# Kernel tuning notes

Measured on AMD Instinct MI355X. Metric: run time of the kernel, lower is better.

The kernel has to match this reference:

```python
import jax, jax.numpy as jnp
import numpy as np
from jax import lax

B, CIN, COUT, K = 256, 3, 16, 3
D, H, W_ = 16, 32, 32
POOL = 4


def setup_inputs() -> dict:
    key = jax.random.key(0)
    kx, kw, kb = jax.random.split(key, 3)
    x = jax.random.normal(kx, (B, CIN, D, H, W_), dtype=jnp.float32)
    # Conv3d default init scale ~ 1/sqrt(fan_in)
    fan_in = CIN * K * K * K
    bound = 1.0 / np.sqrt(fan_in)
    W = jax.random.uniform(kw, (COUT, CIN, K, K, K), dtype=jnp.float32, minval=-bound, maxval=bound)
    b = jax.random.uniform(kb, (COUT,), dtype=jnp.float32, minval=-bound, maxval=bound)
    return {"x": x, "W": W, "b": b}


def reference(x, W, b):
    # Conv3d, valid padding, stride 1: [B,16,14,30,30]
    y = lax.conv_general_dilated(
        x, W, window_strides=(1, 1, 1), padding="VALID",
        dimension_numbers=("NCDHW", "OIDHW", "NCDHW"))
    y = y + b[None, :, None, None, None]
    # channel softmax (dim=1)
    s = jax.nn.softmax(y, axis=1)
    # 4x4x4 max-pool, stride 4, no padding: [B,16,3,7,7]
    out = lax.reduce_window(
        s, -jnp.inf, lax.max,
        window_dimensions=(1, 1, POOL, POOL, POOL),
        window_strides=(1, 1, POOL, POOL, POOL),
        padding="VALID")
    return out
```

## Files before the change

### kernel.cpp

```cpp
#include <hip/hip_runtime.h>
#include <math.h>

#define BATCH 256
#define CIN   3
#define COUT  16
#define DI    16
#define HI    32
#define WI    32

typedef _Float16 f16;
typedef f16   f16x4 __attribute__((ext_vector_type(4)));
typedef f16   f16x8 __attribute__((ext_vector_type(8)));
typedef float f32x4 __attribute__((ext_vector_type(4)));

#define LOG2E 1.44269504088896340736f

#define ROWU   144
#define PLANEU 4320
#define XS_N   (6 * PLANEU)
#define G8OFF  (2 * PLANEU + 2 * ROWU)

#define SV8(a, b) __builtin_shufflevector(a, b, 0, 1, 2, 3, 4, 5, 6, 7)
#define MFMA16(A, B, C) __builtin_amdgcn_mfma_f32_16x16x32_f16(A, B, C, 0, 0, 0)

#define DPPMAX(v, ctrl) do {                                                  \
    int t_ = __builtin_amdgcn_update_dpp(                                     \
        0, __builtin_bit_cast(int, v), (ctrl), 0xF, 0xF, false);              \
    v = fmaxf(v, __builtin_bit_cast(float, t_));                              \
} while (0)

__global__ __launch_bounds__(640, 8) void conv_sm_pool_mfma(
    const float* __restrict__ x, const float* __restrict__ W,
    const float* __restrict__ bias, float* __restrict__ out)
{
    __shared__ __align__(16) f16 xs[XS_N];

    const int tid  = threadIdx.x;
    const int lane = tid & 63;
    const int wave = tid >> 6;
    const int b    = blockIdx.x / 3;
    const int pd   = blockIdx.x % 3;
    const int d0   = pd * 4;

    const int col = lane & 15;
    const int kq  = lane >> 4;

    const float* wc  = W + col * 81;
    const float* wqp = wc + kq * 6;
    f16x8 wm[3];
    #pragma unroll
    for (int kw = 0; kw < 3; ++kw) {
        #pragma unroll
        for (int j = 0; j < 8; ++j) {
            const int ci = j & 3, jj = j >> 2;
            float v = (ci < 3) ? wqp[ci * 27 + 3 * jj + kw] * LOG2E : 0.f;
            wm[kw][j] = (f16)v;
        }
    }
    f16x8 wg = {};
    if (kq == 0) {
        #pragma unroll
        for (int j = 0; j < 8; ++j) {
            const int ci = j & 3, kw = j >> 2;
            if (ci < 3) wg[j] = (f16)(wc[ci * 27 + 24 + kw] * LOG2E);
        }
    } else if (kq == 1) {
        #pragma unroll
        for (int j = 0; j < 3; ++j) wg[j] = (f16)(wc[j * 27 + 26] * LOG2E);
    }
    const float4 braw = *(const float4*)(bias + kq * 4);
    float4 bv;
    bv.x = braw.x * LOG2E; bv.y = braw.y * LOG2E;
    bv.z = braw.z * LOG2E; bv.w = braw.w * LOG2E;

    for (int i = tid; i < 1440; i += 640) {
        int wqd = i & 7;
        int r   = i >> 3;
        int hh  = r % 30;
        int dd  = r / 30;
        const float* px = x + ((size_t)b * 48 + (d0 + dd)) * 1024 + hh * 32 + wqd * 4;
        float4 a0 = *(const float4*)(px);
        float4 a1 = *(const float4*)(px + 16384);
        float4 a2 = *(const float4*)(px + 32768);
        f16x8 p0, p1;
        p0[0] = (f16)a0.x; p0[1] = (f16)a1.x; p0[2] = (f16)a2.x; p0[3] = (f16)0.f;
        p0[4] = (f16)a0.y; p0[5] = (f16)a1.y; p0[6] = (f16)a2.y; p0[7] = (f16)0.f;
        p1[0] = (f16)a0.z; p1[1] = (f16)a1.z; p1[2] = (f16)a2.z; p1[3] = (f16)0.f;
        p1[4] = (f16)a0.w; p1[5] = (f16)a1.w; p1[6] = (f16)a2.w; p1[7] = (f16)0.f;
        f16* dst = xs + ((dd * 30 + hh) * 36 + wqd * 4) * 4;
        *(f16x8*)(dst)     = p0;
        *(f16x8*)(dst + 8) = p1;
    }

    const int g0   = kq * 2;
    const int off1 = (g0 / 3) * PLANEU + (g0 % 3) * ROWU;
    const int off2 = ((g0 + 1) / 3) * PLANEU + ((g0 + 1) % 3) * ROWU;
    const int hl = col >> 2, wl = col & 3;
    const int spat  = hl * ROWU + wl * 4;

    __syncthreads();

    for (int c = wave; c < 49; c += 10) {
        const int ch = c / 7;
        const int pw = c - ch * 7;
        const f16* base = xs + ch * 4 * ROWU + pw * 16 + spat;
        const f16* a1 = base + off1;
        const f16* a2 = base + off2;
        const f16* a3 = base + G8OFF;

        f32x4 acc[4];
        #pragma unroll
        for (int d = 0; d < 4; ++d) {
            const int dp = d * PLANEU;
            f16x4 b10 = *(const f16x4*)(a1 + dp);
            f16x4 b20 = *(const f16x4*)(a2 + dp);
            f16x4 b11 = *(const f16x4*)(a1 + dp + 4);
            f16x4 b21 = *(const f16x4*)(a2 + dp + 4);
            f16x4 b12 = *(const f16x4*)(a1 + dp + 8);
            f16x4 b22 = *(const f16x4*)(a2 + dp + 8);
            f16x4 ga = b10, gb = b11;
            if (kq == 0) {
                ga = *(const f16x4*)(a3 + dp);
                gb = *(const f16x4*)(a3 + dp + 4);
            } else if (kq == 1) {
                ga = *(const f16x4*)(a3 + dp + 8);
            }

            __builtin_amdgcn_s_setprio(1);
            f32x4 a_ = {0.f, 0.f, 0.f, 0.f};
            a_ = MFMA16(wm[0], SV8(b10, b20), a_);
            a_ = MFMA16(wm[1], SV8(b11, b21), a_);
            a_ = MFMA16(wm[2], SV8(b12, b22), a_);
            a_ = MFMA16(wg,    SV8(ga,  gb),  a_);
            __builtin_amdgcn_s_setprio(0);
            acc[d] = a_;
        }

        float ev[4][4], s[4];
        #pragma unroll
        for (int d = 0; d < 4; ++d) {
            float y0 = acc[d][0] + bv.x, y1 = acc[d][1] + bv.y;
            float y2 = acc[d][2] + bv.z, y3 = acc[d][3] + bv.w;
            ev[d][0] = __builtin_amdgcn_exp2f(y0);
            ev[d][1] = __builtin_amdgcn_exp2f(y1);
            ev[d][2] = __builtin_amdgcn_exp2f(y2);
            ev[d][3] = __builtin_amdgcn_exp2f(y3);
            s[d] = (ev[d][0] + ev[d][1]) + (ev[d][2] + ev[d][3]);
        }
        #pragma unroll
        for (int d = 0; d < 4; ++d) s[d] += __shfl_xor(s[d], 16);
        #pragma unroll
        for (int d = 0; d < 4; ++d) s[d] += __shfl_xor(s[d], 32);

        f32x4 pm = {0.f, 0.f, 0.f, 0.f};
        #pragma unroll
        for (int d = 0; d < 4; ++d) {
            float iv = __builtin_amdgcn_rcpf(s[d]);
            pm[0] = fmaxf(pm[0], ev[d][0] * iv);
            pm[1] = fmaxf(pm[1], ev[d][1] * iv);
            pm[2] = fmaxf(pm[2], ev[d][2] * iv);
            pm[3] = fmaxf(pm[3], ev[d][3] * iv);
        }

        #pragma unroll
        for (int r = 0; r < 4; ++r) {
            float v = pm[r];
            DPPMAX(v, 0x128);
            DPPMAX(v, 0x124);
            DPPMAX(v, 0x122);
            DPPMAX(v, 0x121);
            pm[r] = v;
        }

        if (col == 0) {
            float* po = out + ((size_t)b * COUT + kq * 4) * 147 + pd * 49 + c;
            po[0]   = pm[0];
            po[147] = pm[1];
            po[294] = pm[2];
            po[441] = pm[3];
        }
    }
}

extern "C" void kernel_launch(void* const* d_in, const int* in_sizes, int n_in,
                              void* d_out, int out_size, void* d_ws, size_t ws_size,
                              hipStream_t stream) {
    const float* x    = (const float*)d_in[0];
    const float* W    = (const float*)d_in[1];
    const float* bias = (const float*)d_in[2];
    float* out = (float*)d_out;

    conv_sm_pool_mfma<<<BATCH * 3, 640, 0, stream>>>(x, W, bias, out);
}
```

Before: 33.35 us.

## Split each block along H into two halves with 512 threads and smaller LDS

Each (batch, depth-slab) work item is now split into two workgroups covering output H rows 0-3 and 4-6, loading 18 or 14 input rows instead of 30. The LDS buffer shrinks, the block size drops to 512 threads, and the grid doubles. The intent is more resident blocks and better load balance across CUs, with a swizzled block index so paired halves land near each other. The change also drops the setprio hints and the kq-conditional loads for the extra MFMA operand, which now reads unconditionally. The cost is redundant halo loads (rows 16-17 are fetched by both halves) and more per-block setup.

```diff
diff --git a/kernel.cpp b/kernel.cpp
--- a/kernel.cpp
+++ b/kernel.cpp
@@ -16,7 +16,7 @@
 #define LOG2E 1.44269504088896340736f
 
 #define ROWU   144
-#define PLANEU 4320
+#define PLANEU (18 * ROWU)
 #define XS_N   (6 * PLANEU)
 #define G8OFF  (2 * PLANEU + 2 * ROWU)
 
@@ -29,7 +29,7 @@
     v = fmaxf(v, __builtin_bit_cast(float, t_));                              \
 } while (0)
 
-__global__ __launch_bounds__(640, 8) void conv_sm_pool_mfma(
+__global__ __launch_bounds__(512, 8) void conv_sm_pool_mfma(
     const float* __restrict__ x, const float* __restrict__ W,
     const float* __restrict__ bias, float* __restrict__ out)
 {
@@ -38,9 +38,15 @@
     const int tid  = threadIdx.x;
     const int lane = tid & 63;
     const int wave = tid >> 6;
-    const int b    = blockIdx.x / 3;
-    const int pd   = blockIdx.x % 3;
-    const int d0   = pd * 4;
+
+    const int wgid = blockIdx.x;
+    const int hc = (wgid >> 3) & 1;
+    const int p  = ((wgid >> 4) << 3) | (wgid & 7);
+    const int b  = p / 3;
+    const int pd = p % 3;
+    const int d0 = pd * 4;
+    const int row0  = hc ? 16 : 0;
+    const int nrows = hc ? 14 : 18;
 
     const int col = lane & 15;
     const int kq  = lane >> 4;
@@ -73,12 +79,14 @@
     bv.x = braw.x * LOG2E; bv.y = braw.y * LOG2E;
     bv.z = braw.z * LOG2E; bv.w = braw.w * LOG2E;
 
-    for (int i = tid; i < 1440; i += 640) {
+    const int nitems = 6 * nrows * 8;
+    for (int i = tid; i < nitems; i += 512) {
         int wqd = i & 7;
         int r   = i >> 3;
-        int hh  = r % 30;
-        int dd  = r / 30;
-        const float* px = x + ((size_t)b * 48 + (d0 + dd)) * 1024 + hh * 32 + wqd * 4;
+        int hh  = r % nrows;
+        int dd  = r / nrows;
+        const float* px = x + ((size_t)b * 48 + (d0 + dd)) * 1024
+                            + (row0 + hh) * 32 + wqd * 4;
         float4 a0 = *(const float4*)(px);
         float4 a1 = *(const float4*)(px + 16384);
         float4 a2 = *(const float4*)(px + 32768);
@@ -87,7 +95,7 @@
         p0[4] = (f16)a0.y; p0[5] = (f16)a1.y; p0[6] = (f16)a2.y; p0[7] = (f16)0.f;
         p1[0] = (f16)a0.z; p1[1] = (f16)a1.z; p1[2] = (f16)a2.z; p1[3] = (f16)0.f;
         p1[4] = (f16)a0.w; p1[5] = (f16)a1.w; p1[6] = (f16)a2.w; p1[7] = (f16)0.f;
-        f16* dst = xs + ((dd * 30 + hh) * 36 + wqd * 4) * 4;
+        f16* dst = xs + (dd * 18 + hh) * ROWU + wqd * 16;
         *(f16x8*)(dst)     = p0;
         *(f16x8*)(dst + 8) = p1;
     }
@@ -97,16 +105,18 @@
     const int off2 = ((g0 + 1) / 3) * PLANEU + ((g0 + 1) % 3) * ROWU;
     const int hl = col >> 2, wl = col & 3;
     const int spat  = hl * ROWU + wl * 4;
+    const int g8sel = (kq == 0) ? 0 : 8;
 
     __syncthreads();
 
-    for (int c = wave; c < 49; c += 10) {
-        const int ch = c / 7;
-        const int pw = c - ch * 7;
-        const f16* base = xs + ch * 4 * ROWU + pw * 16 + spat;
+    const int ncell = hc ? 21 : 28;
+    for (int c = wave; c < ncell; c += 8) {
+        const int chl = c / 7;
+        const int pw  = c - chl * 7;
+        const f16* base = xs + chl * 4 * ROWU + pw * 16 + spat;
         const f16* a1 = base + off1;
         const f16* a2 = base + off2;
-        const f16* a3 = base + G8OFF;
+        const f16* a3 = base + G8OFF + g8sel;
 
         f32x4 acc[4];
         #pragma unroll
@@ -118,21 +128,13 @@
             f16x4 b21 = *(const f16x4*)(a2 + dp + 4);
             f16x4 b12 = *(const f16x4*)(a1 + dp + 8);
             f16x4 b22 = *(const f16x4*)(a2 + dp + 8);
-            f16x4 ga = b10, gb = b11;
-            if (kq == 0) {
-                ga = *(const f16x4*)(a3 + dp);
-                gb = *(const f16x4*)(a3 + dp + 4);
-            } else if (kq == 1) {
-                ga = *(const f16x4*)(a3 + dp + 8);
-            }
-
-            __builtin_amdgcn_s_setprio(1);
+            f16x4 ga  = *(const f16x4*)(a3 + dp);
+            f16x4 gb  = *(const f16x4*)(a3 + dp + 4);
             f32x4 a_ = {0.f, 0.f, 0.f, 0.f};
             a_ = MFMA16(wm[0], SV8(b10, b20), a_);
             a_ = MFMA16(wm[1], SV8(b11, b21), a_);
             a_ = MFMA16(wm[2], SV8(b12, b22), a_);
             a_ = MFMA16(wg,    SV8(ga,  gb),  a_);
-            __builtin_amdgcn_s_setprio(0);
             acc[d] = a_;
         }
 
@@ -173,7 +175,8 @@
         }
 
         if (col == 0) {
-            float* po = out + ((size_t)b * COUT + kq * 4) * 147 + pd * 49 + c;
+            const int ch = hc ? 4 + chl : chl;
+            float* po = out + ((size_t)b * COUT + kq * 4) * 147 + pd * 49 + ch * 7 + pw;
             po[0]   = pm[0];
             po[147] = pm[1];
             po[294] = pm[2];
@@ -190,5 +193,5 @@
     const float* bias = (const float*)d_in[2];
     float* out = (float*)d_out;
 
-    conv_sm_pool_mfma<<<BATCH * 3, 640, 0, stream>>>(x, W, bias, out);
+    conv_sm_pool_mfma<<<BATCH * 3 * 2, 512, 0, stream>>>(x, W, bias, out);
 }
```

New measurement: 32.81 us. Within noise of the previous version (-1.6%).
